# Optimization experiments

Hardware: AMD Instinct MI355X
Metric: run time of the kernel (lower is better)

The kernel has to match this reference:

```python
import jax, jax.numpy as jnp
import numpy as np

H = 512  # hidden_size
D = 512  # embed_dim == input_size
V = 50000  # embed_num
B, S = 64, 256
C = 5  # class_num


def setup_inputs() -> dict:
    key = jax.random.key(0)
    ks = jax.random.split(key, 8)
    sc_in = 1.0 / np.sqrt(D + H)
    return {
        "x": jax.random.randint(ks[0], (B, S), 0, V),
        "embed": jax.random.normal(ks[1], (V, D), dtype=jnp.float32) * 0.02,
        # gate order: [f, i, c, o]; each gate Linear(D+H -> H)
        "fwd_W": jax.random.normal(ks[2], (4, H, D + H), dtype=jnp.float32) * sc_in,
        "fwd_b": jax.random.normal(ks[3], (4, H), dtype=jnp.float32) * sc_in,
        "bwd_W": jax.random.normal(ks[4], (4, H, D + H), dtype=jnp.float32) * sc_in,
        "bwd_b": jax.random.normal(ks[5], (4, H), dtype=jnp.float32) * sc_in,
        "Wout": jax.random.normal(ks[6], (C, H), dtype=jnp.float32) * (1.0 / np.sqrt(H)),
        "bout": jax.random.normal(ks[7], (C,), dtype=jnp.float32) * 0.01,
    }


def _lstm_scan(xs, W, b):
    # xs: [S, B, D]; W: [4, H, D+H]; b: [4, H]
    Bsz = xs.shape[1]
    h0 = jnp.zeros((Bsz, H), xs.dtype)
    c0 = jnp.zeros((Bsz, H), xs.dtype)

    def step(carry, xt):
        h, c = carry
        z = jnp.concatenate([xt, h], axis=1)              # [B, D+H]
        gates = jnp.einsum('bk,ghk->gbh', z, W) + b[:, None, :]  # [4, B, H]
        f = jax.nn.sigmoid(gates[0])
        i = jax.nn.sigmoid(gates[1])
        ctil = jnp.tanh(gates[2])
        o = jax.nn.sigmoid(gates[3])
        # faithful to source: ct = f*ctil + i*ctil (prev cell state unused)
        c_new = (f + i) * ctil
        h_new = o * jnp.tanh(c_new)
        return (h_new, c_new), h_new

    _, hs = jax.lax.scan(step, (h0, c0), xs)
    return hs  # [S, B, H]


def reference(x, embed, fwd_W, fwd_b, bwd_W, bwd_b, Wout, bout):
    xe = embed[x]                      # [B, S, D]
    xs = jnp.transpose(xe, (1, 0, 2))  # [S, B, D]
    h_fwd = _lstm_scan(xs, fwd_W, fwd_b)                        # [S, B, H]
    h_bwd = _lstm_scan(xs[::-1], bwd_W, bwd_b)[::-1]            # aligned [S, B, H]
    combined = h_fwd * h_bwd           # elementwise product, per source
    pooled = jnp.max(jnp.tanh(combined), axis=0)  # max over time -> [B, H]
    return pooled @ Wout.T + bout      # [B, C]
```

## Files before the change

kernel.cpp:

```cpp
#include <hip/hip_runtime.h>
#include <math.h>

#define HH 512
#define DD 512
#define BB 64
#define SS 256
#define KK 1024
#define CC 5

typedef __attribute__((ext_vector_type(8))) short short8;
typedef __attribute__((ext_vector_type(4))) float float4v;

#define OFF_XEF     0u
#define OFF_ROT     33554432u
#define ROT_SLOT_B  262144u
#define OFF_FLG     100925440u
#define OFF_POOLED  0u

__device__ __forceinline__ unsigned f2bf_bits(float f) {
    unsigned u = __builtin_bit_cast(unsigned, f);
    return (u + 0x7fffu + ((u >> 16) & 1u)) >> 16;
}
__device__ __forceinline__ float sigm_(float v) {
    return 1.f / (1.f + expf(-v));
}
__device__ __forceinline__ float tanh_(float v) {
    return tanhf(v);
}

__global__ __launch_bounds__(256)
void gather_split_k(const int* __restrict__ x, const float* __restrict__ embed,
                    short* __restrict__ xef)
{
    const int s   = blockIdx.x;
    const int tid = threadIdx.x;
    const int b   = tid & 63;
    const int seg = tid >> 6;
    __shared__ int rows[BB];
    if (tid < BB) rows[tid] = x[tid * SS + s];
    __syncthreads();
    const float* e = embed + (size_t)rows[b] * DD + seg * 128;
    short* oh = xef + ((size_t)(s * 2 + 0) * BB + b) * 512 + seg * 128;
    short* ol = xef + ((size_t)(s * 2 + 1) * BB + b) * 512 + seg * 128;
    for (int k0 = 0; k0 < 128; k0 += 8) {
        const float4 a = *(const float4*)(e + k0);
        const float4 c = *(const float4*)(e + k0 + 4);
        const float ev[8] = {a.x, a.y, a.z, a.w, c.x, c.y, c.z, c.w};
        short8 vh, vl;
        #pragma unroll
        for (int j = 0; j < 8; ++j) {
            const unsigned hib = f2bf_bits(ev[j]);
            const float hif = __builtin_bit_cast(float, hib << 16);
            const unsigned lob = f2bf_bits(ev[j] - hif);
            vh[j] = (short)hib;
            vl[j] = (short)lob;
        }
        *(short8*)(oh + k0) = vh;
        *(short8*)(ol + k0) = vl;
    }
}

__global__ __launch_bounds__(256)
void zero_k(unsigned* __restrict__ base, int ndw)
{
    int i = blockIdx.x * 256 + threadIdx.x;
    const int stride = gridDim.x * 256;
    for (; i < ndw; i += stride) base[i] = 0u;
}

__global__ void __launch_bounds__(256, 1)
bilstm_recur_k(const short* __restrict__ xef,
               const float* __restrict__ fwd_W, const float* __restrict__ bwd_W,
               const float* __restrict__ fwd_b, const float* __restrict__ bwd_b,
               short* __restrict__ rot, unsigned* __restrict__ flg)
{
    extern __shared__ char smem[];
    short8* wlds = (short8*)smem;
    char*   hbuf = smem + 65536;
    float*  ex   = (float*)(smem + 131072);
    unsigned short* stg = (unsigned short*)(smem + 135168);

    const int w      = blockIdx.x;
    const int dir    = w >> 7;
    const int wlocal = w & 127;
    const int h0     = wlocal << 2;
    const int tid    = threadIdx.x;
    const int lane   = tid & 63;
    const int wv     = __builtin_amdgcn_readfirstlane(tid >> 6);
    const int n0     = wv << 4;
    const int nn     = lane & 15;
    const int quad   = lane >> 4;

    {
        const float* W = dir ? bwd_W : fwd_W;
        const int m  = lane & 15;
        const int g  = m >> 2;
        const int hh = m & 3;
        const float* wrow = W + ((size_t)g * HH + h0 + hh) * KK + quad * 8;
        for (int kk = 0; kk < 8; ++kk) {
            const int kt = wv * 8 + kk;
            const float4 a  = *(const float4*)(wrow + kt * 32);
            const float4 c4 = *(const float4*)(wrow + kt * 32 + 4);
            const float ev[8] = {a.x, a.y, a.z, a.w, c4.x, c4.y, c4.z, c4.w};
            short8 vh, vl;
            #pragma unroll
            for (int j = 0; j < 8; ++j) {
                const unsigned hib = f2bf_bits(ev[j]);
                const float hif = __builtin_bit_cast(float, hib << 16);
                const unsigned lob = f2bf_bits(ev[j] - hif);
                vh[j] = (short)hib;
                vl[j] = (short)lob;
            }
            wlds[(0 * 32 + kt) * 64 + lane] = vh;
            wlds[(1 * 32 + kt) * 64 + lane] = vl;
        }
    }
    __syncthreads();

    const float* bi = dir ? bwd_b : fwd_b;
    const float4 biasv = *(const float4*)(bi + quad * HH + h0);
    const float bias_arr[4] = {biasv.x, biasv.y, biasv.z, biasv.w};

    unsigned* myflg = flg + dir * 128;
    float* exw = ex + wv * 256;
    const int b = n0 + nn;

    for (int t = 0; t < SS; ++t) {
        const int s = dir ? (SS - 1 - t) : t;

        float4v acc = {0.f, 0.f, 0.f, 0.f};

        {
            const short8* xh8 = (const short8*)(xef +
                ((size_t)(s * 2 + 0) * BB + b) * 512 + quad * 8);
            const short8* xl8 = (const short8*)(xef +
                ((size_t)(s * 2 + 1) * BB + b) * 512 + quad * 8);
            #pragma unroll
            for (int kt = 0; kt < 16; ++kt) {
                const short8 xh  = xh8[kt * 4];
                const short8 xl  = xl8[kt * 4];
                const short8 whi = wlds[(0 * 32 + kt) * 64 + lane];
                const short8 wlo = wlds[(1 * 32 + kt) * 64 + lane];
                acc = __builtin_amdgcn_mfma_f32_16x16x32_bf16(whi, xh, acc, 0, 0, 0);
                acc = __builtin_amdgcn_mfma_f32_16x16x32_bf16(whi, xl, acc, 0, 0, 0);
                acc = __builtin_amdgcn_mfma_f32_16x16x32_bf16(wlo, xh, acc, 0, 0, 0);
            }
        }

        if (t > 0) {
            const unsigned tgt = (unsigned)t;
            unsigned va, vb;
            va = __hip_atomic_load(myflg + lane, __ATOMIC_RELAXED,
                                   __HIP_MEMORY_SCOPE_AGENT);
            vb = __hip_atomic_load(myflg + 64 + lane, __ATOMIC_RELAXED,
                                   __HIP_MEMORY_SCOPE_AGENT);
            while (__any(va < tgt || vb < tgt)) {
                __builtin_amdgcn_s_sleep(32);
                va = __hip_atomic_load(myflg + lane, __ATOMIC_RELAXED,
                                       __HIP_MEMORY_SCOPE_AGENT);
                vb = __hip_atomic_load(myflg + 64 + lane, __ATOMIC_RELAXED,
                                       __HIP_MEMORY_SCOPE_AGENT);
            }
            asm volatile("" ::: "memory");
        }

        {
            const char* slot = (const char*)rot + (size_t)t * ROT_SLOT_B
                             + (size_t)dir * 65536;
            const short8* hq = (const short8*)(slot);
            const short8* lq = (const short8*)(slot + 131072);

            short8 sh[16], sl[16];
            #pragma unroll
            for (int it = 0; it < 16; ++it)
                sh[it] = hq[it * 256 + tid];
            #pragma unroll
            for (int it = 0; it < 16; ++it)
                sl[it] = lq[it * 256 + tid];

            const int kb = (tid & 63) * 16;
            const int bbb = tid >> 6;

            #pragma unroll
            for (int it = 0; it < 16; ++it) {
                const int bb = it * 4 + bbb;
                *(short8*)(hbuf + ((bb << 10) | (kb ^ ((bb & 7) << 4)))) = sh[it];
            }
            __syncthreads();
            #pragma unroll
            for (int kt = 0; kt < 16; ++kt) {
                const short8 uh = *(const short8*)(hbuf + ((b << 10) |
                    ((quad * 16 + kt * 64) ^ ((b & 7) << 4))));
                const short8 whi = wlds[(0 * 32 + 16 + kt) * 64 + lane];
                const short8 wlo = wlds[(1 * 32 + 16 + kt) * 64 + lane];
                acc = __builtin_amdgcn_mfma_f32_16x16x32_bf16(whi, uh, acc, 0, 0, 0);
                acc = __builtin_amdgcn_mfma_f32_16x16x32_bf16(wlo, uh, acc, 0, 0, 0);
            }
            __syncthreads();

            #pragma unroll
            for (int it = 0; it < 16; ++it) {
                const int bb = it * 4 + bbb;
                *(short8*)(hbuf + ((bb << 10) | (kb ^ ((bb & 7) << 4)))) = sl[it];
            }
            __syncthreads();
            #pragma unroll
            for (int kt = 0; kt < 16; ++kt) {
                const short8 ul = *(const short8*)(hbuf + ((b << 10) |
                    ((quad * 16 + kt * 64) ^ ((b & 7) << 4))));
                const short8 whi = wlds[(0 * 32 + 16 + kt) * 64 + lane];
                acc = __builtin_amdgcn_mfma_f32_16x16x32_bf16(whi, ul, acc, 0, 0, 0);
            }
        }

        #pragma unroll
        for (int r2 = 0; r2 < 4; ++r2)
            exw[(quad * 4 + r2) * 16 + nn] = acc[r2] + bias_arr[r2];
        float pg[4];
        #pragma unroll
        for (int g_ = 0; g_ < 4; ++g_)
            pg[g_] = exw[(g_ * 4 + quad) * 16 + nn];

        const float f_  = sigm_(pg[0]);
        const float i_  = sigm_(pg[1]);
        const float ct  = tanh_(pg[2]);
        const float o_  = sigm_(pg[3]);
        const float c_  = (f_ + i_) * ct;
        const float hn  = o_ * tanh_(c_);

        const unsigned hib = f2bf_bits(hn);
        const float hif = __builtin_bit_cast(float, hib << 16);
        const unsigned lob = f2bf_bits(hn - hif);
        stg[(0 * 4 + quad) * 64 + b] = (unsigned short)hib;
        stg[(1 * 4 + quad) * 64 + b] = (unsigned short)lob;
        __syncthreads();

        {
            const int plane = tid >> 7;
            const int d     = tid & 127;
            const int pb    = d >> 1;
            const int pair  = d & 1;
            const unsigned v0 = stg[(plane * 4 + pair * 2 + 0) * 64 + pb];
            const unsigned v1 = stg[(plane * 4 + pair * 2 + 1) * 64 + pb];
            const unsigned val = v0 | (v1 << 16);
            const size_t so = (size_t)(t + 1) * 131072 + (size_t)plane * 65536
                            + (size_t)dir * 32768 + (size_t)pb * 512
                            + h0 + pair * 2;
            unsigned* dst = (unsigned*)(rot + so);
            __hip_atomic_store(dst, val, __ATOMIC_RELAXED,
                               __HIP_MEMORY_SCOPE_AGENT);
        }
        asm volatile("s_waitcnt vmcnt(0)" ::: "memory");
        __syncthreads();
        if (tid == 0)
            __hip_atomic_store(myflg + wlocal, (unsigned)(t + 1),
                               __ATOMIC_RELAXED, __HIP_MEMORY_SCOPE_AGENT);
    }
}

__global__ __launch_bounds__(256)
void pool_k(const short* __restrict__ rot, float* __restrict__ pooled)
{
    const int tg = blockIdx.x * 256 + threadIdx.x;
    const int b  = tg >> 9;
    const int h  = tg & 511;
    const int off = b * 512 + h;
    float m = -2.0f;
    for (int s = 0; s < SS; ++s) {
        const short* fs = rot + (size_t)(s + 1) * 131072;
        const short* bs = rot + (size_t)(SS - s) * 131072;
        const unsigned hf = (unsigned short)fs[off];
        const unsigned lf = (unsigned short)fs[65536 + off];
        const unsigned hb = (unsigned short)bs[32768 + off];
        const unsigned lb = (unsigned short)bs[65536 + 32768 + off];
        const float af = __builtin_bit_cast(float, hf << 16)
                       + __builtin_bit_cast(float, lf << 16);
        const float ab = __builtin_bit_cast(float, hb << 16)
                       + __builtin_bit_cast(float, lb << 16);
        m = fmaxf(m, tanhf(af * ab));
    }
    pooled[(size_t)h * BB + b] = m;
}

__global__ __launch_bounds__(256)
void outgemm_k(const float* __restrict__ pooled, const float* __restrict__ Wout,
               const float* __restrict__ bout, float* __restrict__ out)
{
    const int c   = blockIdx.x;
    const int tid = threadIdx.x;
    const int b   = tid & 63;
    const int q   = __builtin_amdgcn_readfirstlane(tid >> 6);
    float p = 0.0f;
    for (int j = 0; j < 128; ++j) {
        const int h = q * 128 + j;
        p = fmaf(pooled[(size_t)h * BB + b], Wout[c * HH + h], p);
    }
    __shared__ float red[4][BB];
    red[q][b] = p;
    __syncthreads();
    if (tid < BB)
        out[tid * CC + c] = red[0][tid] + red[1][tid] + red[2][tid] + red[3][tid] + bout[c];
}

extern "C" void kernel_launch(void* const* d_in, const int* in_sizes, int n_in,
                              void* d_out, int out_size, void* d_ws, size_t ws_size,
                              hipStream_t stream)
{
    const int*   x     = (const int*)d_in[0];
    const float* embed = (const float*)d_in[1];
    const float* fwd_W = (const float*)d_in[2];
    const float* fwd_b = (const float*)d_in[3];
    const float* bwd_W = (const float*)d_in[4];
    const float* bwd_b = (const float*)d_in[5];
    const float* Wout  = (const float*)d_in[6];
    const float* bout  = (const float*)d_in[7];
    float* out = (float*)d_out;

    char* wsb = (char*)d_ws;
    short*    xef    = (short*)(wsb + OFF_XEF);
    short*    rot    = (short*)(wsb + OFF_ROT);
    unsigned* flg    = (unsigned*)(wsb + OFF_FLG);
    float*    pooled = (float*)(wsb + OFF_POOLED);

    gather_split_k<<<SS, 256, 0, stream>>>(x, embed, xef);
    zero_k<<<64, 256, 0, stream>>>((unsigned*)(wsb + OFF_ROT),
                                   (int)(ROT_SLOT_B / 4));
    zero_k<<<1, 256, 0, stream>>>(flg, 256);

    hipFuncSetAttribute((const void*)bilstm_recur_k,
                        hipFuncAttributeMaxDynamicSharedMemorySize, 136192);
    void* args[] = {(void*)&xef, (void*)&fwd_W, (void*)&bwd_W,
                    (void*)&fwd_b, (void*)&bwd_b,
                    (void*)&rot, (void*)&flg};
    hipLaunchCooperativeKernel((void*)bilstm_recur_k, dim3(256), dim3(256),
                               args, 136192, stream);

    pool_k<<<128, 256, 0, stream>>>(rot, pooled);
    outgemm_k<<<CC, 256, 0, stream>>>(pooled, Wout, bout, out);
}
```

Measured before the change: 2.147 ms.

## Make each wave stage only its own batch rows to drop block barriers

Each wave now loads and writes to LDS only the 16 batch rows of the recurrent state it consumes, instead of the whole block cooperatively staging all 64 rows. This removes three __syncthreads per timestep in the recurrent matmul, plus one in the output staging, which now uses a per-wave buffer. The cost is redundant global loads when several waves share the same rows, and each wave's LDS writes now rely on being visible to its own lanes without a block barrier.

Result: faster. 2.034 ms (-5.3%).

```diff
diff --git a/kernel.cpp b/kernel.cpp
--- a/kernel.cpp
+++ b/kernel.cpp
@@ -123,6 +123,7 @@
 
     unsigned* myflg = flg + dir * 128;
     float* exw = ex + wv * 256;
+    unsigned short* stgw = stg + wv * 128;
     const int b = n0 + nn;
 
     for (int t = 0; t < SS; ++t) {
@@ -173,20 +174,17 @@
             short8 sh[16], sl[16];
             #pragma unroll
             for (int it = 0; it < 16; ++it)
-                sh[it] = hq[it * 256 + tid];
+                sh[it] = hq[(n0 + it) * 64 + lane];
             #pragma unroll
             for (int it = 0; it < 16; ++it)
-                sl[it] = lq[it * 256 + tid];
-
-            const int kb = (tid & 63) * 16;
-            const int bbb = tid >> 6;
+                sl[it] = lq[(n0 + it) * 64 + lane];
 
             #pragma unroll
             for (int it = 0; it < 16; ++it) {
-                const int bb = it * 4 + bbb;
-                *(short8*)(hbuf + ((bb << 10) | (kb ^ ((bb & 7) << 4)))) = sh[it];
-            }
-            __syncthreads();
+                const int r = n0 + it;
+                *(short8*)(hbuf + ((r << 10) |
+                    ((lane * 16) ^ ((r & 7) << 4)))) = sh[it];
+            }
             #pragma unroll
             for (int kt = 0; kt < 16; ++kt) {
                 const short8 uh = *(const short8*)(hbuf + ((b << 10) |
@@ -196,14 +194,13 @@
                 acc = __builtin_amdgcn_mfma_f32_16x16x32_bf16(whi, uh, acc, 0, 0, 0);
                 acc = __builtin_amdgcn_mfma_f32_16x16x32_bf16(wlo, uh, acc, 0, 0, 0);
             }
-            __syncthreads();
 
             #pragma unroll
             for (int it = 0; it < 16; ++it) {
-                const int bb = it * 4 + bbb;
-                *(short8*)(hbuf + ((bb << 10) | (kb ^ ((bb & 7) << 4)))) = sl[it];
-            }
-            __syncthreads();
+                const int r = n0 + it;
+                *(short8*)(hbuf + ((r << 10) |
+                    ((lane * 16) ^ ((r & 7) << 4)))) = sl[it];
+            }
             #pragma unroll
             for (int kt = 0; kt < 16; ++kt) {
                 const short8 ul = *(const short8*)(hbuf + ((b << 10) |
@@ -231,19 +228,18 @@
         const unsigned hib = f2bf_bits(hn);
         const float hif = __builtin_bit_cast(float, hib << 16);
         const unsigned lob = f2bf_bits(hn - hif);
-        stg[(0 * 4 + quad) * 64 + b] = (unsigned short)hib;
-        stg[(1 * 4 + quad) * 64 + b] = (unsigned short)lob;
-        __syncthreads();
+        stgw[0 * 64 + quad * 16 + nn] = (unsigned short)hib;
+        stgw[1 * 64 + quad * 16 + nn] = (unsigned short)lob;
 
         {
-            const int plane = tid >> 7;
-            const int d     = tid & 127;
-            const int pb    = d >> 1;
-            const int pair  = d & 1;
-            const unsigned v0 = stg[(plane * 4 + pair * 2 + 0) * 64 + pb];
-            const unsigned v1 = stg[(plane * 4 + pair * 2 + 1) * 64 + pb];
+            const int pl   = lane >> 5;
+            const int pair = (lane >> 4) & 1;
+            const int n2   = lane & 15;
+            const int pb   = n0 + n2;
+            const unsigned v0 = stgw[pl * 64 + (pair * 2 + 0) * 16 + n2];
+            const unsigned v1 = stgw[pl * 64 + (pair * 2 + 1) * 16 + n2];
             const unsigned val = v0 | (v1 << 16);
-            const size_t so = (size_t)(t + 1) * 131072 + (size_t)plane * 65536
+            const size_t so = (size_t)(t + 1) * 131072 + (size_t)pl * 65536
                             + (size_t)dir * 32768 + (size_t)pb * 512
                             + h0 + pair * 2;
             unsigned* dst = (unsigned*)(rot + so);
```
